# Performance work log

Hardware: AMD Instinct MI355X
Metric: run time of the kernel (lower is better)

The kernel has to match this reference:

```python
import jax, jax.numpy as jnp
import numpy as np
from jax import lax

B = 8192
C = 16          # conv_channels
H = 256         # hidden_size = W_init.shape[0]
OUT = 10
IN_SIZE = C * 14 * 14  # 3136


def setup_inputs() -> dict:
    key = jax.random.key(0)
    ks = jax.random.split(key, 8)
    x = jax.random.normal(ks[0], (B, 1, 28, 28), dtype=jnp.float32)
    conv_w = jax.random.normal(ks[1], (C, 1, 3, 3), dtype=jnp.float32) * 0.1
    conv_b = jax.random.normal(ks[2], (C,), dtype=jnp.float32) * 0.1
    W_in = jax.random.normal(ks[3], (H, IN_SIZE), dtype=jnp.float32) * 0.02
    b_in = jax.random.normal(ks[4], (H,), dtype=jnp.float32) * 0.02
    W_out = jax.random.normal(ks[5], (OUT, H), dtype=jnp.float32) * 0.05
    b_out = jax.random.normal(ks[6], (OUT,), dtype=jnp.float32) * 0.05
    # register_buffer('W', W_init * 1e-5)
    W = jax.random.normal(ks[7], (H, H), dtype=jnp.float32) * 1e-5
    return {"x": x, "conv_w": conv_w, "conv_b": conv_b, "W_in": W_in,
            "b_in": b_in, "W_out": W_out, "b_out": b_out, "W": W}


def reference(x, conv_w, conv_b, W_in, b_in, W_out, b_out, W):
    # Conv2d(1, C, 3, padding=1) + ReLU
    y = lax.conv_general_dilated(
        x, conv_w, window_strides=(1, 1), padding="SAME",
        dimension_numbers=("NCHW", "OIHW", "NCHW"))
    y = jax.nn.relu(y + conv_b[None, :, None, None])
    # MaxPool2d(2): 28x28 -> 14x14
    y = lax.reduce_window(y, -jnp.inf, lax.max,
                          (1, 1, 2, 2), (1, 1, 2, 2), "VALID")
    conv_flat = y.reshape(y.shape[0], -1)  # [B, C*14*14], NCHW order matches torch view
    # step 0: E_t = Linear(conv_flat); r_t starts at zeros
    E0 = conv_flat @ W_in.T + b_in            # [B, H]
    r = jax.nn.relu(E0)                       # relu(0 @ W + E0 + 0)
    # 9 more steps with zero input -> E_t = b_in
    for _ in range(9):
        r = jax.nn.relu(r @ W + b_in + r)
    return r @ W_out.T + b_out                # [B, 10]
```

## Files before the change

kernel.cpp:

```cpp
#include <hip/hip_runtime.h>

typedef _Float16 f16x8 __attribute__((ext_vector_type(8)));
typedef _Float16 f16x4 __attribute__((ext_vector_type(4)));
typedef _Float16 h2   __attribute__((ext_vector_type(2)));
typedef float f32x4 __attribute__((ext_vector_type(4)));

__device__ __forceinline__ void gload16(const void* g, void* l) {
  __builtin_amdgcn_global_load_lds(
      (__attribute__((address_space(1))) void*)g,
      (__attribute__((address_space(3))) void*)l, 16, 0, 0);
}

#define W_SCALE 4096.0f
#define W_UNSCALE (1.0f / 4096.0f)

#define ISL(row, k) (((row) >> 4) * 50176 + ((k) >> 5) * 512 + \
                     ((((k) >> 3) & 3) << 7) + (((row) & 15) << 3) + ((k) & 7))

__global__ __launch_bounds__(256) void conv_pool_kernel(
    const float* __restrict__ x,
    const float* __restrict__ cw,
    const float* __restrict__ cb,
    _Float16* __restrict__ out) {
  __shared__ float img[30 * 32];
  __shared__ h2 wsm[144];
  __shared__ h2 bsm[16];
  int tid = threadIdx.x;
  for (int i = tid; i < 960; i += 256) img[i] = 0.f;
  if (tid < 144) { float w = cw[tid]; wsm[tid] = h2{(_Float16)w, (_Float16)w}; }
  if (tid < 16)  { float b = cb[tid]; bsm[tid] = h2{(_Float16)b, (_Float16)b}; }
  __syncthreads();
  if (tid < 196) {
    float4 v = *(const float4*)(x + (size_t)blockIdx.x * 784 + tid * 4);
    int row = tid / 7, col4 = (tid - row * 7) * 4;
    float* dst = img + (row + 1) * 32 + col4 + 1;
    dst[0] = v.x; dst[1] = v.y; dst[2] = v.z; dst[3] = v.w;
  }
  __syncthreads();
  if (tid >= 196) return;
  int ph = tid / 14, pw = tid - ph * 14;
  const float* base = img + (2 * ph) * 32 + (2 * pw);
  h2 xp[4][3];
#pragma unroll
  for (int i = 0; i < 4; ++i) {
    float r0 = base[i * 32 + 0], r1 = base[i * 32 + 1];
    float r2 = base[i * 32 + 2], r3 = base[i * 32 + 3];
    xp[i][0] = h2{(_Float16)r0, (_Float16)r1};
    xp[i][1] = h2{(_Float16)r1, (_Float16)r2};
    xp[i][2] = h2{(_Float16)r2, (_Float16)r3};
  }
  _Float16* orow = out + (size_t)blockIdx.x * 3136 + tid;
#pragma unroll
  for (int ch = 0; ch < 16; ++ch) {
    h2 a01 = bsm[ch], a23 = bsm[ch];
#pragma unroll
    for (int i = 0; i < 3; ++i)
#pragma unroll
      for (int j = 0; j < 3; ++j) {
        h2 wv = wsm[ch * 9 + i * 3 + j];
        a01 = __builtin_elementwise_fma(wv, xp[i][j], a01);
        a23 = __builtin_elementwise_fma(wv, xp[i + 1][j], a23);
      }
    h2 m2 = __builtin_elementwise_max(a01, a23);
    _Float16 m = m2[0] > m2[1] ? m2[0] : m2[1];
    m = m > (_Float16)0.f ? m : (_Float16)0.f;
    orow[ch * 196] = m;
  }
}

__global__ __launch_bounds__(256) void win_cvt_kernel(
    const float* __restrict__ in,
    _Float16* __restrict__ out) {
  int n = blockIdx.x, tid = threadIdx.x;
  const float* src = in + (size_t)n * 3136;
#pragma unroll
  for (int it = 0; it < 4; ++it) {
    int idx = it * 256 + tid;
    if (idx < 784) {
      int k0 = idx * 4;
      float4 v = *(const float4*)(src + k0);
      f16x4 h = {(_Float16)v.x, (_Float16)v.y, (_Float16)v.z, (_Float16)v.w};
      *(f16x4*)(out + ISL(n, k0)) = h;
    }
  }
}

__global__ void wt_cvt_kernel(const float* __restrict__ W,
                              _Float16* __restrict__ Wt) {
  int i = blockIdx.x * 256 + threadIdx.x;
  int k = i >> 8, n = i & 255;
  Wt[n * 256 + k] = (_Float16)(W[k * 256 + n] * W_SCALE);
}

__global__ __launch_bounds__(256) void gemm1_kernel(
    const _Float16* __restrict__ A,
    const _Float16* __restrict__ Bw,
    float* __restrict__ Z) {
  __shared__ __align__(16) _Float16 As[2048];
  __shared__ __align__(16) _Float16 Bs[2048];
  int tid = threadIdx.x, lane = tid & 63, wid = tid >> 6;
  int bm = blockIdx.x * 64, bn = blockIdx.y * 64;
  int k0 = blockIdx.z * 1568;
  f32x4 acc[2][2];
#pragma unroll
  for (int i = 0; i < 2; ++i)
#pragma unroll
    for (int j = 0; j < 2; ++j) acc[i][j] = (f32x4){0.f, 0.f, 0.f, 0.f};

  int ar = tid >> 2;
  const _Float16* Ag = A + (size_t)(bm + ar) * 3136 + k0 + (tid & 3) * 8;
  _Float16* asw = As + (ar >> 4) * 512 + (tid & 3) * 128 + (ar & 15) * 8;
  const _Float16* Bg = Bw + ((bn >> 4) + wid) * 50176 + (k0 >> 5) * 512 + lane * 8;
  _Float16* bsw = Bs + wid * 512;

  int rko = ((lane >> 4) << 7) + ((lane & 15) << 3);
  int ga = (wid & 1) * 2, gb = (wid >> 1) * 2;

  f16x8 areg = *(const f16x8*)Ag;
  for (int t = 0; t < 49; ++t) {
    __syncthreads();
    *(f16x8*)asw = areg;
    gload16(Bg + t * 512, bsw);
    if (t < 48) areg = *(const f16x8*)(Ag + (t + 1) * 32);
    __syncthreads();
    f16x8 af0 = *(const f16x8*)(As + (ga + 0) * 512 + rko);
    f16x8 af1 = *(const f16x8*)(As + (ga + 1) * 512 + rko);
    f16x8 bf0 = *(const f16x8*)(Bs + (gb + 0) * 512 + rko);
    f16x8 bf1 = *(const f16x8*)(Bs + (gb + 1) * 512 + rko);
    acc[0][0] = __builtin_amdgcn_mfma_f32_16x16x32_f16(af0, bf0, acc[0][0], 0, 0, 0);
    acc[0][1] = __builtin_amdgcn_mfma_f32_16x16x32_f16(af0, bf1, acc[0][1], 0, 0, 0);
    acc[1][0] = __builtin_amdgcn_mfma_f32_16x16x32_f16(af1, bf0, acc[1][0], 0, 0, 0);
    acc[1][1] = __builtin_amdgcn_mfma_f32_16x16x32_f16(af1, bf1, acc[1][1], 0, 0, 0);
  }
  float* Zp = Z + (size_t)blockIdx.z * 8192 * 256;
  int wm = (wid & 1) * 32, wn = (wid >> 1) * 32;
  int rg = (lane >> 4) * 4, cl = lane & 15;
#pragma unroll
  for (int mi = 0; mi < 2; ++mi)
#pragma unroll
    for (int ni = 0; ni < 2; ++ni)
#pragma unroll
      for (int j = 0; j < 4; ++j) {
        int m = bm + wm + mi * 16 + rg + j;
        int n = bn + wn + ni * 16 + cl;
        Zp[(size_t)m * 256 + n] = acc[mi][ni][j];
      }
}

__global__ __launch_bounds__(512, 2) void rnn_persist_kernel(
    const float*    __restrict__ Z0,
    const float*    __restrict__ Z1,
    const _Float16* __restrict__ Wt,
    const float*    __restrict__ b_in,
    const float*    __restrict__ Wo,
    const float*    __restrict__ bo,
    float*          __restrict__ out)
{
  __shared__ __align__(16) _Float16 r_lds[32 * 256];
  int tid = threadIdx.x, lane = tid & 63, wid = tid >> 6;
  int wr = wid >> 2, wc = wid & 3;
  int bm = blockIdx.x * 32;

  f16x8 wfr[8][4];
#pragma unroll
  for (int kk = 0; kk < 8; ++kk)
#pragma unroll
    for (int ni = 0; ni < 4; ++ni) {
      int n = wc * 64 + ni * 16 + (lane & 15);
      int kpos = kk * 32 + (lane >> 4) * 8;
      wfr[kk][ni] = *(const f16x8*)(Wt + n * 256 + kpos);
    }

  float breg[4];
  float rres[4][4];
  int rrow = wr * 16 + (lane >> 4) * 4;
#pragma unroll
  for (int ni = 0; ni < 4; ++ni) {
    int col = wc * 64 + ni * 16 + (lane & 15);
    breg[ni] = b_in[col];
#pragma unroll
    for (int j = 0; j < 4; ++j) {
      size_t idx = (size_t)(bm + rrow + j) * 256 + col;
      rres[ni][j] = fmaxf(Z0[idx] + Z1[idx] + breg[ni], 0.f);
    }
  }

#pragma unroll
  for (int it = 0; it < 2; ++it) {
    int idx = it * 512 + tid;
    int row = idx >> 5;
    int kc = (idx & 31) * 8;
    size_t off = (size_t)(bm + row) * 256 + kc;
    f32x4 a0 = *(const f32x4*)(Z0 + off);
    f32x4 a1 = *(const f32x4*)(Z0 + off + 4);
    f32x4 b0 = *(const f32x4*)(Z1 + off);
    f32x4 b1 = *(const f32x4*)(Z1 + off + 4);
    f32x4 c0 = *(const f32x4*)(b_in + kc);
    f32x4 c1 = *(const f32x4*)(b_in + kc + 4);
    f16x8 h;
#pragma unroll
    for (int j = 0; j < 4; ++j) h[j] = (_Float16)fmaxf(a0[j] + b0[j] + c0[j], 0.f);
#pragma unroll
    for (int j = 0; j < 4; ++j) h[4 + j] = (_Float16)fmaxf(a1[j] + b1[j] + c1[j], 0.f);
    *(f16x8*)(r_lds + row * 256 + (kc ^ ((row & 7) << 3))) = h;
  }

  int arow = wr * 16 + (lane & 15);
  int aswz = (arow & 7) << 3;
  for (int s = 0; s < 9; ++s) {
    __syncthreads();
    f32x4 acc[4];
#pragma unroll
    for (int ni = 0; ni < 4; ++ni) acc[ni] = (f32x4){0.f, 0.f, 0.f, 0.f};
#pragma unroll
    for (int kk = 0; kk < 8; ++kk) {
      int kpos = kk * 32 + (lane >> 4) * 8;
      f16x8 af = *(const f16x8*)(r_lds + arow * 256 + (kpos ^ aswz));
#pragma unroll
      for (int ni = 0; ni < 4; ++ni)
        acc[ni] = __builtin_amdgcn_mfma_f32_16x16x32_f16(af, wfr[kk][ni], acc[ni], 0, 0, 0);
    }
    __syncthreads();
#pragma unroll
    for (int ni = 0; ni < 4; ++ni) {
      int col = wc * 64 + ni * 16 + (lane & 15);
#pragma unroll
      for (int j = 0; j < 4; ++j) {
        float v = fmaxf(fmaf(acc[ni][j], W_UNSCALE, breg[ni] + rres[ni][j]), 0.f);
        rres[ni][j] = v;
        int row = rrow + j;
        r_lds[row * 256 + (col ^ ((row & 7) << 3))] = (_Float16)v;
      }
    }
  }
  __syncthreads();

  if (tid < 320) {
    int row = tid / 10, o = tid - row * 10;
    int rswz = (row & 7) << 3;
    float accd = 0.f;
    for (int kc = 0; kc < 256; kc += 8) {
      f16x8 rv = *(const f16x8*)(r_lds + row * 256 + (kc ^ rswz));
      const float* wp = Wo + o * 256 + kc;
#pragma unroll
      for (int j = 0; j < 8; ++j) accd = fmaf((float)rv[j], wp[j], accd);
    }
    out[(size_t)(bm + row) * 10 + o] = accd + bo[o];
  }
}

extern "C" void kernel_launch(void* const* d_in, const int* in_sizes, int n_in,
                              void* d_out, int out_size, void* d_ws, size_t ws_size,
                              hipStream_t stream) {
  const float* x      = (const float*)d_in[0];
  const float* conv_w = (const float*)d_in[1];
  const float* conv_b = (const float*)d_in[2];
  const float* W_in   = (const float*)d_in[3];
  const float* b_in   = (const float*)d_in[4];
  const float* W_out  = (const float*)d_in[5];
  const float* b_out  = (const float*)d_in[6];
  const float* W      = (const float*)d_in[7];
  float* out = (float*)d_out;

  char* ws = (char*)d_ws;
  size_t o = 0;
  _Float16* conv_flat = (_Float16*)(ws + o); o += (size_t)8192 * 3136 * 2;
  _Float16* W_in_h    = (_Float16*)(ws + o); o += (size_t)256 * 3136 * 2;
  _Float16* Wt_h      = (_Float16*)(ws + o); o += (size_t)256 * 256 * 2;
  float*    Z01       = (float*)(ws + o);    o += (size_t)2 * 8192 * 256 * 4;

  win_cvt_kernel<<<256, 256, 0, stream>>>(W_in, W_in_h);
  wt_cvt_kernel<<<256, 256, 0, stream>>>(W, Wt_h);
  conv_pool_kernel<<<8192, 256, 0, stream>>>(x, conv_w, conv_b, conv_flat);
  gemm1_kernel<<<dim3(128, 4, 2), 256, 0, stream>>>(conv_flat, W_in_h, Z01);
  rnn_persist_kernel<<<256, 512, 0, stream>>>(Z01, Z01 + (size_t)8192 * 256,
                                              Wt_h, b_in, W_out, b_out, out);
}
```

Measured before the change: 166.8 us.

## Double-buffer gemm1 with direct LDS loads, widen N tile, merge prep kernels

The first GEMM now loads both A and B tiles straight from global memory into LDS and double-buffers them, so the next k-slice is fetched while MFMAs run on the current one. This drops one of the two barriers per iteration and removes the register staging of A. The N tile grows from 64 to 128, so each block does twice the MFMAs per A load and the fp16 conv activations are re-read from memory half as often. The two weight-conversion kernels are merged into one launch to save launch overhead. In exchange the kernel uses more LDS, holds more accumulator registers, and launches half as many blocks, which could lower occupancy.

Result: no change. 168.2 us (+0.9%).

```diff
diff --git a/kernel.cpp b/kernel.cpp
--- a/kernel.cpp
+++ b/kernel.cpp
@@ -68,77 +68,84 @@
   }
 }
 
-__global__ __launch_bounds__(256) void win_cvt_kernel(
-    const float* __restrict__ in,
-    _Float16* __restrict__ out) {
-  int n = blockIdx.x, tid = threadIdx.x;
-  const float* src = in + (size_t)n * 3136;
-#pragma unroll
-  for (int it = 0; it < 4; ++it) {
-    int idx = it * 256 + tid;
-    if (idx < 784) {
-      int k0 = idx * 4;
-      float4 v = *(const float4*)(src + k0);
-      f16x4 h = {(_Float16)v.x, (_Float16)v.y, (_Float16)v.z, (_Float16)v.w};
-      *(f16x4*)(out + ISL(n, k0)) = h;
-    }
-  }
-}
-
-__global__ void wt_cvt_kernel(const float* __restrict__ W,
-                              _Float16* __restrict__ Wt) {
-  int i = blockIdx.x * 256 + threadIdx.x;
-  int k = i >> 8, n = i & 255;
-  Wt[n * 256 + k] = (_Float16)(W[k * 256 + n] * W_SCALE);
+__global__ __launch_bounds__(256) void prep_kernel(
+    const float* __restrict__ W_in, _Float16* __restrict__ W_in_h,
+    const float* __restrict__ W, _Float16* __restrict__ Wt) {
+  int b = blockIdx.x, tid = threadIdx.x;
+  if (b < 256) {
+    const float* src = W_in + (size_t)b * 3136;
+#pragma unroll
+    for (int it = 0; it < 4; ++it) {
+      int idx = it * 256 + tid;
+      if (idx < 784) {
+        int k0 = idx * 4;
+        float4 v = *(const float4*)(src + k0);
+        f16x4 h = {(_Float16)v.x, (_Float16)v.y, (_Float16)v.z, (_Float16)v.w};
+        *(f16x4*)(W_in_h + ISL(b, k0)) = h;
+      }
+    }
+  } else {
+    int i = (b - 256) * 256 + tid;
+    int k = i >> 8, n = i & 255;
+    Wt[n * 256 + k] = (_Float16)(W[k * 256 + n] * W_SCALE);
+  }
 }
 
 __global__ __launch_bounds__(256) void gemm1_kernel(
     const _Float16* __restrict__ A,
     const _Float16* __restrict__ Bw,
     float* __restrict__ Z) {
-  __shared__ __align__(16) _Float16 As[2048];
-  __shared__ __align__(16) _Float16 Bs[2048];
+  __shared__ __align__(16) _Float16 As[2][2048];
+  __shared__ __align__(16) _Float16 Bs[2][4096];
   int tid = threadIdx.x, lane = tid & 63, wid = tid >> 6;
-  int bm = blockIdx.x * 64, bn = blockIdx.y * 64;
+  int bm = blockIdx.x * 64, bn = blockIdx.y * 128;
   int k0 = blockIdx.z * 1568;
-  f32x4 acc[2][2];
+  f32x4 acc[2][4];
 #pragma unroll
   for (int i = 0; i < 2; ++i)
 #pragma unroll
-    for (int j = 0; j < 2; ++j) acc[i][j] = (f32x4){0.f, 0.f, 0.f, 0.f};
-
-  int ar = tid >> 2;
-  const _Float16* Ag = A + (size_t)(bm + ar) * 3136 + k0 + (tid & 3) * 8;
-  _Float16* asw = As + (ar >> 4) * 512 + (tid & 3) * 128 + (ar & 15) * 8;
-  const _Float16* Bg = Bw + ((bn >> 4) + wid) * 50176 + (k0 >> 5) * 512 + lane * 8;
-  _Float16* bsw = Bs + wid * 512;
+    for (int j = 0; j < 4; ++j) acc[i][j] = (f32x4){0.f, 0.f, 0.f, 0.f};
+
+  const _Float16* Ag  = A + (size_t)(bm + wid * 16 + (lane & 15)) * 3136
+                          + k0 + ((lane >> 4) << 3);
+  const _Float16* Bg0 = Bw + (size_t)((bn >> 4) + 2 * wid) * 50176
+                          + ((k0 >> 5) << 9) + lane * 8;
+  const _Float16* Bg1 = Bg0 + 50176;
 
   int rko = ((lane >> 4) << 7) + ((lane & 15) << 3);
-  int ga = (wid & 1) * 2, gb = (wid >> 1) * 2;
-
-  f16x8 areg = *(const f16x8*)Ag;
+  int ga = (wid & 1) * 2, gb = (wid >> 1) * 4;
+
+  gload16(Ag,  &As[0][wid * 512]);
+  gload16(Bg0, &Bs[0][2 * wid * 512]);
+  gload16(Bg1, &Bs[0][2 * wid * 512 + 512]);
+  __syncthreads();
+
+  int cur = 0;
   for (int t = 0; t < 49; ++t) {
+    if (t < 48) {
+      gload16(Ag + (t + 1) * 32,            &As[cur ^ 1][wid * 512]);
+      gload16(Bg0 + (size_t)(t + 1) * 512,  &Bs[cur ^ 1][2 * wid * 512]);
+      gload16(Bg1 + (size_t)(t + 1) * 512,  &Bs[cur ^ 1][2 * wid * 512 + 512]);
+    }
+    f16x8 af0 = *(const f16x8*)(&As[cur][(ga + 0) * 512 + rko]);
+    f16x8 af1 = *(const f16x8*)(&As[cur][(ga + 1) * 512 + rko]);
+#pragma unroll
+    for (int ni = 0; ni < 4; ++ni) {
+      f16x8 bf = *(const f16x8*)(&Bs[cur][(gb + ni) * 512 + rko]);
+      acc[0][ni] = __builtin_amdgcn_mfma_f32_16x16x32_f16(af0, bf, acc[0][ni], 0, 0, 0);
+      acc[1][ni] = __builtin_amdgcn_mfma_f32_16x16x32_f16(af1, bf, acc[1][ni], 0, 0, 0);
+    }
     __syncthreads();
-    *(f16x8*)asw = areg;
-    gload16(Bg + t * 512, bsw);
-    if (t < 48) areg = *(const f16x8*)(Ag + (t + 1) * 32);
-    __syncthreads();
-    f16x8 af0 = *(const f16x8*)(As + (ga + 0) * 512 + rko);
-    f16x8 af1 = *(const f16x8*)(As + (ga + 1) * 512 + rko);
-    f16x8 bf0 = *(const f16x8*)(Bs + (gb + 0) * 512 + rko);
-    f16x8 bf1 = *(const f16x8*)(Bs + (gb + 1) * 512 + rko);
-    acc[0][0] = __builtin_amdgcn_mfma_f32_16x16x32_f16(af0, bf0, acc[0][0], 0, 0, 0);
-    acc[0][1] = __builtin_amdgcn_mfma_f32_16x16x32_f16(af0, bf1, acc[0][1], 0, 0, 0);
-    acc[1][0] = __builtin_amdgcn_mfma_f32_16x16x32_f16(af1, bf0, acc[1][0], 0, 0, 0);
-    acc[1][1] = __builtin_amdgcn_mfma_f32_16x16x32_f16(af1, bf1, acc[1][1], 0, 0, 0);
-  }
+    cur ^= 1;
+  }
+
   float* Zp = Z + (size_t)blockIdx.z * 8192 * 256;
-  int wm = (wid & 1) * 32, wn = (wid >> 1) * 32;
+  int wm = (wid & 1) * 32, wn = (wid >> 1) * 64;
   int rg = (lane >> 4) * 4, cl = lane & 15;
 #pragma unroll
   for (int mi = 0; mi < 2; ++mi)
 #pragma unroll
-    for (int ni = 0; ni < 2; ++ni)
+    for (int ni = 0; ni < 4; ++ni)
 #pragma unroll
       for (int j = 0; j < 4; ++j) {
         int m = bm + wm + mi * 16 + rg + j;
@@ -269,10 +276,9 @@
   _Float16* Wt_h      = (_Float16*)(ws + o); o += (size_t)256 * 256 * 2;
   float*    Z01       = (float*)(ws + o);    o += (size_t)2 * 8192 * 256 * 4;
 
-  win_cvt_kernel<<<256, 256, 0, stream>>>(W_in, W_in_h);
-  wt_cvt_kernel<<<256, 256, 0, stream>>>(W, Wt_h);
+  prep_kernel<<<512, 256, 0, stream>>>(W_in, W_in_h, W, Wt_h);
   conv_pool_kernel<<<8192, 256, 0, stream>>>(x, conv_w, conv_b, conv_flat);
-  gemm1_kernel<<<dim3(128, 4, 2), 256, 0, stream>>>(conv_flat, W_in_h, Z01);
+  gemm1_kernel<<<dim3(128, 2, 2), 256, 0, stream>>>(conv_flat, W_in_h, Z01);
   rnn_persist_kernel<<<256, 512, 0, stream>>>(Z01, Z01 + (size_t)8192 * 256,
                                               Wt_h, b_in, W_out, b_out, out);
 }
```
